# Kernel tuning notes

Measured on AMD Instinct MI355X. Metric: run time of the kernel, lower is better.

The kernel has to match this reference:

```python
import jax, jax.numpy as jnp
from jax import lax
import numpy as np

N, C, H, W = 8, 256, 96, 96
K = 5            # d_conv=4 forced odd -> 5 in FauxScan1D
HID = 2 * C      # ff_mult * dim


def setup_inputs() -> dict:
    key = jax.random.key(0)
    ks = iter(jax.random.split(key, 40))
    nrm = lambda *s: jax.random.normal(next(ks), s, jnp.float32) * 0.02
    inp = {'x': jax.random.normal(next(ks), (N, C, H, W), jnp.float32)}
    inp['ln1_w'] = jnp.ones((C,), jnp.float32)
    inp['ln1_b'] = jnp.zeros((C,), jnp.float32)
    inp['dw_w'] = nrm(3, 3, 1, C)   # depthwise 3x3, HWIO with feature_group_count=C
    inp['dw_b'] = jnp.zeros((C,), jnp.float32)
    for d in ('lr', 'rl', 'tb', 'bt'):
        inp[d + '_dw_w'] = nrm(K, 1, C)   # depthwise conv1d, WIO
        inp[d + '_dw_b'] = jnp.zeros((C,), jnp.float32)
        inp[d + '_g_w'] = nrm(C, C)       # 1x1 gate conv (out, in)
        inp[d + '_g_b'] = jnp.zeros((C,), jnp.float32)
    inp['fuse_w'] = nrm(C, C)
    inp['fuse_b'] = jnp.zeros((C,), jnp.float32)
    inp['ln2_w'] = jnp.ones((C,), jnp.float32)
    inp['ln2_b'] = jnp.zeros((C,), jnp.float32)
    inp['ff1_w'] = nrm(2 * HID, C)
    inp['ff1_b'] = jnp.zeros((2 * HID,), jnp.float32)
    inp['ff2_w'] = nrm(C, HID)
    inp['ff2_b'] = jnp.zeros((C,), jnp.float32)
    return inp


def _ln2d(x, w, b, eps=1e-6):
    # LayerNorm2d: per-(sample, channel) stats over H,W
    m = x.mean(axis=(2, 3), keepdims=True)
    v = ((x - m) ** 2).mean(axis=(2, 3), keepdims=True)
    return (x - m) * lax.rsqrt(v + eps) * w[None, :, None, None] + b[None, :, None, None]


def _scan1d(seq, dw_w, dw_b, g_w, g_b):
    # FauxScan1D: seq (B, L, C) -> dwconv1d(k=5, pad=2) * sigmoid(pointwise gate)
    c = seq.shape[-1]
    y = lax.conv_general_dilated(seq, dw_w, (1,), [(K // 2, K // 2)],
                                 dimension_numbers=('NWC', 'WIO', 'NWC'),
                                 feature_group_count=c) + dw_b
    g = jax.nn.sigmoid(jnp.einsum('blc,dc->bld', seq, g_w) + g_b)
    return y * g


def _forward(x, ln1_w, ln1_b, dw_w, dw_b,
             lr_dw_w, lr_dw_b, lr_g_w, lr_g_b,
             rl_dw_w, rl_dw_b, rl_g_w, rl_g_b,
             tb_dw_w, tb_dw_b, tb_g_w, tb_g_b,
             bt_dw_w, bt_dw_b, bt_g_w, bt_g_b,
             fuse_w, fuse_b, ln2_w, ln2_b, ff1_w, ff1_b, ff2_w, ff2_b):
    n, c, hh, ww = x.shape
    y = _ln2d(x, ln1_w, ln1_b)
    y = lax.conv_general_dilated(y, dw_w, (1, 1), [(1, 1), (1, 1)],
                                 dimension_numbers=('NCHW', 'HWIO', 'NCHW'),
                                 feature_group_count=c) + dw_b[None, :, None, None]
    y = jnp.transpose(y, (0, 2, 3, 1))  # NHWC
    # lr: rows as sequences
    o = _scan1d(y.reshape(n * hh, ww, c), lr_dw_w, lr_dw_b, lr_g_w, lr_g_b).reshape(n, hh, ww, c)
    # rl: flip width, scan, flip back
    yf = jnp.flip(y, 2).reshape(n * hh, ww, c)
    o = o + jnp.flip(_scan1d(yf, rl_dw_w, rl_dw_b, rl_g_w, rl_g_b).reshape(n, hh, ww, c), 2)
    # tb: columns as sequences
    yt = jnp.transpose(y, (0, 2, 1, 3)).reshape(n * ww, hh, c)
    o = o + jnp.transpose(_scan1d(yt, tb_dw_w, tb_dw_b, tb_g_w, tb_g_b).reshape(n, ww, hh, c), (0, 2, 1, 3))
    # bt: flip height, columns, scan, undo
    yb = jnp.transpose(jnp.flip(y, 1), (0, 2, 1, 3)).reshape(n * ww, hh, c)
    o = o + jnp.flip(jnp.transpose(_scan1d(yb, bt_dw_w, bt_dw_b, bt_g_w, bt_g_b).reshape(n, ww, hh, c), (0, 2, 1, 3)), 1)
    y = jnp.transpose(o, (0, 3, 1, 2))  # back to NCHW
    y = jnp.einsum('nchw,dc->ndhw', y, fuse_w) + fuse_b[None, :, None, None]
    x = x + y
    z = _ln2d(x, ln2_w, ln2_b)
    z = jnp.einsum('nchw,dc->ndhw', z, ff1_w) + ff1_b[None, :, None, None]
    a, g = jnp.split(z, 2, axis=1)  # GLU on channel dim
    z = a * jax.nn.sigmoid(g)
    z = jnp.einsum('nchw,dc->ndhw', z, ff2_w) + ff2_b[None, :, None, None]
    return x + z


def reference(x, ln1_w, ln1_b, dw_w, dw_b,
              lr_dw_w, lr_dw_b, lr_g_w, lr_g_b,
              rl_dw_w, rl_dw_b, rl_g_w, rl_g_b,
              tb_dw_w, tb_dw_b, tb_g_w, tb_g_b,
              bt_dw_w, bt_dw_b, bt_g_w, bt_g_b,
              fuse_w, fuse_b, ln2_w, ln2_b, ff1_w, ff1_b, ff2_w, ff2_b):
    return _forward(x, ln1_w, ln1_b, dw_w, dw_b,
                    lr_dw_w, lr_dw_b, lr_g_w, lr_g_b,
                    rl_dw_w, rl_dw_b, rl_g_w, rl_g_b,
                    tb_dw_w, tb_dw_b, tb_g_w, tb_g_b,
                    bt_dw_w, bt_dw_b, bt_g_w, bt_g_b,
                    fuse_w, fuse_b, ln2_w, ln2_b, ff1_w, ff1_b, ff2_w, ff2_b)
```

## Files before the change

### kernel.cpp

```cpp
#include <hip/hip_runtime.h>

#define TPB 256
#define HWSZ 9216

typedef __attribute__((ext_vector_type(8))) short short8x;
typedef __attribute__((ext_vector_type(4))) float f32x4;
typedef unsigned short ushort_t;
typedef unsigned int uint_t;

__device__ __forceinline__ float sigf(float v) { return 1.0f / (1.0f + __expf(-v)); }

__device__ __forceinline__ ushort_t f2bf(float f) {
  uint_t u = __float_as_uint(f);
  u = (u + 0x7fffu + ((u >> 16) & 1u)) >> 16;
  return (ushort_t)u;
}
__device__ __forceinline__ float bf2f(ushort_t h) {
  return __uint_as_float(((uint_t)h) << 16);
}

__device__ __forceinline__ int swz32(int p, int c) {
  return p * 1024 + ((((c * 4) ^ ((p & 7) << 4)) ^ (((p >> 3) & 3) << 2)));
}

__global__ __launch_bounds__(TPB) void k_pack(
    const float* __restrict__ lrg, const float* __restrict__ rlg,
    const float* __restrict__ tbg, const float* __restrict__ btg,
    const float* __restrict__ fusew, const float* __restrict__ ff1w,
    const float* __restrict__ ff2w,
    ushort_t* __restrict__ Gp, ushort_t* __restrict__ Ftp,
    ushort_t* __restrict__ W1p, ushort_t* __restrict__ W2p) {
  int i = blockIdx.x * TPB + threadIdx.x;
  if (i < 262144) {
    int d = i >> 16, r = i & 65535;
    int kt = r >> 13, nt = (r >> 9) & 15, l = (r >> 3) & 63, j = r & 7;
    int k = kt * 32 + (l >> 4) * 8 + j;
    int n_ = nt * 16 + (l & 15);
    const float* g = (d == 0) ? lrg : (d == 1) ? rlg : (d == 2) ? tbg : btg;
    Gp[i] = f2bf(g[n_ * 256 + k]);
  } else if (i < 327680) {
    int r = i - 262144;
    int kt = r >> 13, nt = (r >> 9) & 15, l = (r >> 3) & 63, j = r & 7;
    int k = kt * 32 + (l >> 4) * 8 + j;
    int n_ = nt * 16 + (l & 15);
    Ftp[r] = f2bf(fusew[n_ * 256 + k]);
  } else if (i < 589824) {
    int r = i - 327680;
    int kt = r >> 15, pb = (r >> 10) & 31, ag = (r >> 9) & 1;
    int l = (r >> 3) & 63, j = r & 7;
    int k = kt * 32 + (l >> 4) * 8 + j;
    int colb = pb * 16 + (l & 15);
    int col = ag ? (512 + colb) : colb;
    W1p[r] = f2bf(ff1w[col * 256 + k]);
  } else if (i < 720896) {
    int r = i - 589824;
    int kt = r >> 13, nt = (r >> 9) & 15, l = (r >> 3) & 63, j = r & 7;
    int k = kt * 32 + (l >> 4) * 8 + j;
    int n_ = nt * 16 + (l & 15);
    W2p[r] = f2bf(ff2w[n_ * 512 + k]);
  }
}

__global__ __launch_bounds__(TPB) void k_stats(const float* __restrict__ src,
                                               float* __restrict__ mean,
                                               float* __restrict__ rstd) {
  int nc = blockIdx.x;
  const float4* p = (const float4*)(src + (long)nc * HWSZ);
  float s = 0.f, s2 = 0.f;
  for (int i = threadIdx.x; i < 2304; i += TPB) {
    float4 v = p[i];
    s += (v.x + v.y) + (v.z + v.w);
    s2 = fmaf(v.x, v.x, fmaf(v.y, v.y, fmaf(v.z, v.z, fmaf(v.w, v.w, s2))));
  }
#pragma unroll
  for (int off = 32; off > 0; off >>= 1) {
    s += __shfl_down(s, off);
    s2 += __shfl_down(s2, off);
  }
  __shared__ float ls[4], ls2[4];
  int lane = threadIdx.x & 63, wv = threadIdx.x >> 6;
  if (lane == 0) { ls[wv] = s; ls2[wv] = s2; }
  __syncthreads();
  if (threadIdx.x == 0) {
    float S = ls[0] + ls[1] + ls[2] + ls[3];
    float S2 = ls2[0] + ls2[1] + ls2[2] + ls2[3];
    float m = S * (1.0f / HWSZ);
    float var = S2 * (1.0f / HWSZ) - m * m;
    mean[nc] = m;
    rstd[nc] = rsqrtf(fmaxf(var, 0.f) + 1e-6f);
  }
}

__global__ __launch_bounds__(TPB) void k_lndw(
    const float* __restrict__ x, const float* __restrict__ mean1,
    const float* __restrict__ rstd1, const float* __restrict__ ln1w,
    const float* __restrict__ ln1b, const float* __restrict__ dww,
    const float* __restrict__ dwb, ushort_t* __restrict__ y,
    ushort_t* __restrict__ yT) {
  __shared__ __align__(16) ushort_t xs[6 * 32 * 104];
  __shared__ __align__(16) ushort_t ot[2 * 96 * 32];
  __shared__ float sc[32], sh[32];

  int tid = threadIdx.x;
  int bid = blockIdx.x;
  int cb = (bid & 7) * 32;
  int hb = (bid >> 3) % 24;
  int n  = bid / 192;
  int h0 = hb * 4;

  if (tid < 32) {
    int c = cb + tid;
    int nc = n * 256 + c;
    float scale = rstd1[nc] * ln1w[c];
    sc[tid] = scale;
    sh[tid] = ln1b[c] - mean1[nc] * scale;
  }
  if (tid < 192) {
    xs[tid * 104 + 3] = 0;
    xs[tid * 104 + 100] = 0;
  }
  __syncthreads();

  for (int i = tid; i < 4608; i += TPB) {
    int rc = i / 24;
    int f4 = i - rc * 24;
    int row = rc >> 5, c = rc & 31;
    int hh = h0 - 1 + row;
    uint2 pk = make_uint2(0, 0);
    if (hh >= 0 && hh < 96) {
      float4 v = *(const float4*)(x + (long)(n * 256 + cb + c) * HWSZ +
                                  hh * 96 + f4 * 4);
      float scale = sc[c], shift = sh[c];
      ushort_t p0 = f2bf(fmaf(v.x, scale, shift));
      ushort_t p1 = f2bf(fmaf(v.y, scale, shift));
      ushort_t p2 = f2bf(fmaf(v.z, scale, shift));
      ushort_t p3 = f2bf(fmaf(v.w, scale, shift));
      pk.x = (uint_t)p0 | ((uint_t)p1 << 16);
      pk.y = (uint_t)p2 | ((uint_t)p3 << 16);
    }
    *(uint2*)(xs + rc * 104 + 4 + f4 * 4) = pk;
  }
  __syncthreads();

  int c = tid & 31, grp = tid >> 5;
  int w0 = grp * 12;
  float wgt[9];
#pragma unroll
  for (int t = 0; t < 9; ++t) wgt[t] = dww[t * 256 + cb + c];
  float bias = dwb[cb + c];

#pragma unroll
  for (int half = 0; half < 2; ++half) {
    float vals[2][12];
#pragma unroll
    for (int sub = 0; sub < 2; ++sub) {
      int orow = half * 2 + sub;
      float R[3][14];
#pragma unroll
      for (int rr = 0; rr < 3; ++rr) {
        const ushort_t* p = xs + ((orow + rr) * 32 + c) * 104;
        R[rr][0] = bf2f(p[3 + w0]);
        ushort4 q0 = *(const ushort4*)(p + 4 + w0);
        ushort4 q1 = *(const ushort4*)(p + 8 + w0);
        ushort4 q2 = *(const ushort4*)(p + 12 + w0);
        R[rr][1] = bf2f(q0.x);  R[rr][2] = bf2f(q0.y);
        R[rr][3] = bf2f(q0.z);  R[rr][4] = bf2f(q0.w);
        R[rr][5] = bf2f(q1.x);  R[rr][6] = bf2f(q1.y);
        R[rr][7] = bf2f(q1.z);  R[rr][8] = bf2f(q1.w);
        R[rr][9] = bf2f(q2.x);  R[rr][10] = bf2f(q2.y);
        R[rr][11] = bf2f(q2.z); R[rr][12] = bf2f(q2.w);
        R[rr][13] = bf2f(p[16 + w0]);
      }
#pragma unroll
      for (int k = 0; k < 12; ++k) {
        float acc = bias;
#pragma unroll
        for (int rr = 0; rr < 3; ++rr) {
          acc = fmaf(R[rr][k], wgt[rr * 3 + 0], acc);
          acc = fmaf(R[rr][k + 1], wgt[rr * 3 + 1], acc);
          acc = fmaf(R[rr][k + 2], wgt[rr * 3 + 2], acc);
        }
        vals[sub][k] = acc;
      }
    }
    if (half == 1) __syncthreads();
#pragma unroll
    for (int sub = 0; sub < 2; ++sub)
#pragma unroll
      for (int k = 0; k < 12; ++k)
        ot[(sub * 96 + w0 + k) * 32 + c] = f2bf(vals[sub][k]);
    __syncthreads();
#pragma unroll
    for (int it = 0; it < 3; ++it) {
      int u = it * 256 + tid;
      int r2 = (u >= 384) ? 1 : 0;
      int rem = u - r2 * 384;
      int w = rem >> 2, cq = rem & 3;
      uint4 v = *(const uint4*)(ot + (r2 * 96 + w) * 32 + cq * 8);
      int h = h0 + half * 2 + r2;
      *(uint4*)(y + ((long)(n * 96 + h) * 96 + w) * 256 + cb + cq * 8) = v;
      *(uint4*)(yT + ((long)(n * 96 + w) * 96 + h) * 256 + cb + cq * 8) = v;
    }
  }
}

__global__ __launch_bounds__(512, 4) void k_scan(
    const ushort_t* __restrict__ src, const uint4* __restrict__ gp4,
    const float* __restrict__ dwaw, const float* __restrict__ dwab,
    const float* __restrict__ gab, const float* __restrict__ dwbw,
    const float* __restrict__ dwbb, const float* __restrict__ gbb,
    ushort_t* __restrict__ dst) {
  __shared__ __align__(16) char pool[34816];
  char* ylds = pool;
  char* olds = pool + 26624;

  int tid = threadIdx.x;
  int bid = blockIdx.x;
  int seg = bid & 1, line = (bid >> 1) % 96, n = bid / 192;
  int p0 = seg * 48;
  long lbase = (long)(n * 96 + line) * 96;

  for (int u = tid; u < 52 * 32; u += 512) {
    int r = u >> 5, ks = u & 31;
    int q = p0 - 2 + r;
    uint4 v = make_uint4(0, 0, 0, 0);
    if (q >= 0 && q < 96)
      v = *(const uint4*)(src + (lbase + q) * 256 + ks * 8);
    *(uint4*)(ylds + r * 512 + ((ks * 16) ^ ((r & 7) << 4))) = v;
  }
  __syncthreads();

  int l = tid & 63, w = tid >> 6;
  int llo = l & 15, lhi = l >> 4;

  float part[3][2][4];

#pragma unroll
  for (int diri = 0; diri < 2; ++diri) {
    f32x4 acc[3][2];
#pragma unroll
    for (int mf = 0; mf < 3; ++mf)
#pragma unroll
      for (int ntl = 0; ntl < 2; ++ntl) acc[mf][ntl] = (f32x4){0.f, 0.f, 0.f, 0.f};

    const uint4* gbase = gp4 + ((long)(diri * 8) * 16 + w * 2) * 64 + l;
    short8x bc0 = *(const short8x*)(gbase);
    short8x bc1 = *(const short8x*)(gbase + 64);
#pragma unroll
    for (int kt = 0; kt < 8; ++kt) {
      short8x bn0, bn1;
      if (kt < 7) {
        bn0 = *(const short8x*)(gbase + (kt + 1) * 1024);
        bn1 = *(const short8x*)(gbase + (kt + 1) * 1024 + 64);
      }
      short8x a[3];
#pragma unroll
      for (int mf = 0; mf < 3; ++mf) {
        int arow = 2 + mf * 16 + llo;
        a[mf] = *(const short8x*)(ylds + arow * 512 +
                                  ((kt * 64 + lhi * 16) ^ ((arow & 7) << 4)));
      }
#pragma unroll
      for (int mf = 0; mf < 3; ++mf) {
        acc[mf][0] = __builtin_amdgcn_mfma_f32_16x16x32_bf16(a[mf], bc0, acc[mf][0], 0, 0, 0);
        acc[mf][1] = __builtin_amdgcn_mfma_f32_16x16x32_bf16(a[mf], bc1, acc[mf][1], 0, 0, 0);
      }
      bc0 = bn0;
      bc1 = bn1;
    }

    const float* dwv = diri ? dwbw : dwaw;
    const float* dbv = diri ? dwbb : dwab;
    const float* gbv = diri ? gbb : gab;
#pragma unroll
    for (int ntl = 0; ntl < 2; ++ntl) {
      int c = (w * 2 + ntl) * 16 + llo;
      float wt[5];
#pragma unroll
      for (int t = 0; t < 5; ++t)
        wt[t] = diri ? dwv[(4 - t) * 256 + c] : dwv[t * 256 + c];
      float cb = dbv[c], gb = gbv[c];
#pragma unroll
      for (int mf = 0; mf < 3; ++mf) {
        int pbase = mf * 16 + lhi * 4;
        float yv[8];
#pragma unroll
        for (int t = 0; t < 8; ++t) {
          int ry = pbase + t;
          yv[t] = bf2f(*(const ushort_t*)(ylds + ry * 512 +
                                          ((c * 2) ^ ((ry & 7) << 4))));
        }
#pragma unroll
        for (int r = 0; r < 4; ++r) {
          float conv = cb;
#pragma unroll
          for (int t = 0; t < 5; ++t) conv = fmaf(yv[r + t], wt[t], conv);
          float val = conv * sigf(acc[mf][ntl][r] + gb);
          if (diri == 0) part[mf][ntl][r] = val;
          else           part[mf][ntl][r] += val;
        }
      }
    }
  }

#pragma unroll
  for (int mf = 0; mf < 3; ++mf) {
    __syncthreads();
#pragma unroll
    for (int ntl = 0; ntl < 2; ++ntl) {
      int c = (w * 2 + ntl) * 16 + llo;
#pragma unroll
      for (int r = 0; r < 4; ++r) {
        int p = lhi * 4 + r;
        *(ushort_t*)(olds + p * 512 + ((c * 2) ^ ((p & 7) << 4))) =
            f2bf(part[mf][ntl][r]);
      }
    }
    __syncthreads();
    {
      int p = tid >> 5, ks = tid & 31;
      uint4 v = *(const uint4*)(olds + p * 512 + ((ks * 16) ^ ((p & 7) << 4)));
      *(uint4*)(dst + (lbase + p0 + mf * 16 + p) * 256 + ks * 8) = v;
    }
  }
}

__global__ __launch_bounds__(512, 4) void k_fuse(
    const ushort_t* __restrict__ o, const ushort_t* __restrict__ oT,
    const ushort_t* __restrict__ Ftp, const float* __restrict__ fuseb,
    const float* __restrict__ x, float* __restrict__ out) {
  __shared__ __align__(16) char pool[24576];

  int tid = threadIdx.x;
  int pix0 = blockIdx.x * 48;
  int n = pix0 / HWSZ, hw0 = pix0 % HWSZ;
  int h = hw0 / 96, w0 = hw0 % 96;

  for (int u = tid; u < 48 * 32; u += 512) {
    int r = u >> 5, ks = u & 31;
    uint4 va = *(const uint4*)(o + (long)(pix0 + r) * 256 + ks * 8);
    uint4 vb = *(const uint4*)(oT + ((long)(n * 96 + w0 + r) * 96 + h) * 256 + ks * 8);
    ushort_t* a8 = (ushort_t*)&va;
    ushort_t* b8 = (ushort_t*)&vb;
#pragma unroll
    for (int j = 0; j < 8; ++j) a8[j] = f2bf(bf2f(a8[j]) + bf2f(b8[j]));
    *(uint4*)(pool + r * 512 + ((ks * 16) ^ ((r & 7) << 4))) = va;
  }
  __syncthreads();

  int l = tid & 63, w = tid >> 6;
  int llo = l & 15, lhi = l >> 4;

  const uint4* fp4 = (const uint4*)Ftp;
  f32x4 acc[3][2];
#pragma unroll
  for (int mf = 0; mf < 3; ++mf)
#pragma unroll
    for (int ntl = 0; ntl < 2; ++ntl) acc[mf][ntl] = (f32x4){0.f, 0.f, 0.f, 0.f};

  const uint4* fbase = fp4 + (long)(w * 2) * 64 + l;
  short8x bc0 = *(const short8x*)(fbase);
  short8x bc1 = *(const short8x*)(fbase + 64);
#pragma unroll
  for (int kt = 0; kt < 8; ++kt) {
    short8x bn0, bn1;
    if (kt < 7) {
      bn0 = *(const short8x*)(fbase + (kt + 1) * 1024);
      bn1 = *(const short8x*)(fbase + (kt + 1) * 1024 + 64);
    }
    short8x a[3];
#pragma unroll
    for (int mf = 0; mf < 3; ++mf) {
      int arow = mf * 16 + llo;
      a[mf] = *(const short8x*)(pool + arow * 512 +
                                ((kt * 64 + lhi * 16) ^ ((arow & 7) << 4)));
    }
#pragma unroll
    for (int mf = 0; mf < 3; ++mf) {
      acc[mf][0] = __builtin_amdgcn_mfma_f32_16x16x32_bf16(a[mf], bc0, acc[mf][0], 0, 0, 0);
      acc[mf][1] = __builtin_amdgcn_mfma_f32_16x16x32_bf16(a[mf], bc1, acc[mf][1], 0, 0, 0);
    }
    bc0 = bn0;
    bc1 = bn1;
  }

#pragma unroll
  for (int mf = 0; mf < 3; ++mf) {
    __syncthreads();
#pragma unroll
    for (int ntl = 0; ntl < 2; ++ntl) {
      int c = (w * 2 + ntl) * 16 + llo;
      float fb = fuseb[c];
#pragma unroll
      for (int r = 0; r < 4; ++r) {
        int p = lhi * 4 + r;
        *(float*)(pool + swz32(p, c)) = acc[mf][ntl][r] + fb;
      }
    }
    __syncthreads();
    for (int i = tid; i < 4096; i += 512) {
      int c = i >> 4, p = i & 15;
      long addr = (long)(n * 256 + c) * HWSZ + hw0 + mf * 16 + p;
      out[addr] = x[addr] + *(const float*)(pool + swz32(p, c));
    }
  }
}

__global__ __launch_bounds__(512, 4) void k_ff1(
    const float* __restrict__ xres, const float* __restrict__ mean2,
    const float* __restrict__ rstd2, const float* __restrict__ ln2w,
    const float* __restrict__ ln2b, const ushort_t* __restrict__ W1p,
    const float* __restrict__ ff1b, ushort_t* __restrict__ u) {
  __shared__ char hA[48 * 512];

  int tid = threadIdx.x;
  int pix0 = blockIdx.x * 48;
  int n = pix0 / HWSZ, hw0 = pix0 % HWSZ;

  for (int i = tid; i < 12288; i += 512) {
    int c = i / 48, p = i % 48;
    int nc = n * 256 + c;
    float v = xres[(long)nc * HWSZ + hw0 + p];
    float hv = (v - mean2[nc]) * rstd2[nc] * ln2w[c] + ln2b[c];
    *(ushort_t*)(hA + p * 512 + ((c * 2) ^ ((p & 7) << 4))) = f2bf(hv);
  }
  __syncthreads();

  int l = tid & 63, w = tid >> 6;
  int llo = l & 15, lhi = l >> 4;

  const uint4* W1p4 = (const uint4*)W1p;
#pragma unroll
  for (int q = 0; q < 4; ++q) {
    int pb = q * 8 + w;
    f32x4 ca[3][2];
#pragma unroll
    for (int mf = 0; mf < 3; ++mf) {
      ca[mf][0] = (f32x4){0.f, 0.f, 0.f, 0.f};
      ca[mf][1] = (f32x4){0.f, 0.f, 0.f, 0.f};
    }
    const uint4* wb = W1p4 + (long)(pb * 2) * 64 + l;
    short8x bca = *(const short8x*)(wb);
    short8x bcg = *(const short8x*)(wb + 64);
#pragma unroll
    for (int kt = 0; kt < 8; ++kt) {
      short8x bna, bng;
      if (kt < 7) {
        bna = *(const short8x*)(wb + (kt + 1) * 4096);
        bng = *(const short8x*)(wb + (kt + 1) * 4096 + 64);
      }
      short8x a[3];
#pragma unroll
      for (int mf = 0; mf < 3; ++mf) {
        int arow = mf * 16 + llo;
        a[mf] = *(const short8x*)(hA + arow * 512 +
                                  ((kt * 64 + lhi * 16) ^ ((arow & 7) << 4)));
      }
#pragma unroll
      for (int mf = 0; mf < 3; ++mf) {
        ca[mf][0] = __builtin_amdgcn_mfma_f32_16x16x32_bf16(a[mf], bca, ca[mf][0], 0, 0, 0);
        ca[mf][1] = __builtin_amdgcn_mfma_f32_16x16x32_bf16(a[mf], bcg, ca[mf][1], 0, 0, 0);
      }
      bca = bna;
      bcg = bng;
    }
    int ucol = pb * 16 + llo;
    float ba = ff1b[ucol], bg = ff1b[512 + ucol];
#pragma unroll
    for (int mf = 0; mf < 3; ++mf)
#pragma unroll
      for (int r = 0; r < 4; ++r) {
        int row = pix0 + mf * 16 + lhi * 4 + r;
        u[(long)row * 512 + ucol] =
            f2bf((ca[mf][0][r] + ba) * sigf(ca[mf][1][r] + bg));
      }
  }
}

__global__ __launch_bounds__(512, 4) void k_ff2(
    const ushort_t* __restrict__ u, const ushort_t* __restrict__ W2p,
    const float* __restrict__ ff2b, float* __restrict__ out) {
  __shared__ __align__(16) char pool[16384];

  int tid = threadIdx.x;
  int pix0 = blockIdx.x * 48;
  int n = pix0 / HWSZ, hw0 = pix0 % HWSZ;

  int l = tid & 63, w = tid >> 6;
  int llo = l & 15, lhi = l >> 4;

  const uint4* W2p4 = (const uint4*)W2p;
  const uint_t* u32 = (const uint_t*)u;

  f32x4 zacc[3][2];
#pragma unroll
  for (int mf = 0; mf < 3; ++mf) {
    zacc[mf][0] = (f32x4){0.f, 0.f, 0.f, 0.f};
    zacc[mf][1] = (f32x4){0.f, 0.f, 0.f, 0.f};
  }

#pragma unroll
  for (int kc = 0; kc < 4; ++kc) {
    __syncthreads();
    for (int i = tid; i < 3072; i += 512) {
      int p = i >> 6, cd = i & 63;
      uint_t v = u32[(long)(pix0 + p) * 256 + kc * 64 + cd];
      *(uint_t*)(pool + p * 256 + ((cd * 4) ^ ((p & 7) << 4))) = v;
    }
    __syncthreads();
#pragma unroll
    for (int ks = 0; ks < 4; ++ks) {
      int kt = kc * 4 + ks;
      short8x a[3];
#pragma unroll
      for (int mf = 0; mf < 3; ++mf) {
        int arow = mf * 16 + llo;
        a[mf] = *(const short8x*)(pool + arow * 256 +
                                  ((ks * 64 + lhi * 16) ^ ((arow & 7) << 4)));
      }
      short8x b0 = *(const short8x*)(W2p4 + (long)(kt * 16 + w * 2) * 64 + l);
      short8x b1 = *(const short8x*)(W2p4 + (long)(kt * 16 + w * 2 + 1) * 64 + l);
#pragma unroll
      for (int mf = 0; mf < 3; ++mf) {
        zacc[mf][0] = __builtin_amdgcn_mfma_f32_16x16x32_bf16(a[mf], b0, zacc[mf][0], 0, 0, 0);
        zacc[mf][1] = __builtin_amdgcn_mfma_f32_16x16x32_bf16(a[mf], b1, zacc[mf][1], 0, 0, 0);
      }
    }
  }

#pragma unroll
  for (int mf = 0; mf < 3; ++mf) {
    __syncthreads();
#pragma unroll
    for (int ntl = 0; ntl < 2; ++ntl) {
      int c = (w * 2 + ntl) * 16 + llo;
      float fb = ff2b[c];
#pragma unroll
      for (int r = 0; r < 4; ++r) {
        int p = lhi * 4 + r;
        *(float*)(pool + swz32(p, c)) = zacc[mf][ntl][r] + fb;
      }
    }
    __syncthreads();
    for (int i = tid; i < 4096; i += 512) {
      int c = i >> 4, p = i & 15;
      long addr = (long)(n * 256 + c) * HWSZ + hw0 + mf * 16 + p;
      out[addr] += *(const float*)(pool + swz32(p, c));
    }
  }
}

extern "C" void kernel_launch(void* const* d_in, const int* in_sizes, int n_in,
                              void* d_out, int out_size, void* d_ws, size_t ws_size,
                              hipStream_t stream) {
  (void)in_sizes; (void)n_in; (void)out_size; (void)ws_size;
  const float* x     = (const float*)d_in[0];
  const float* ln1w  = (const float*)d_in[1];
  const float* ln1b  = (const float*)d_in[2];
  const float* dww   = (const float*)d_in[3];
  const float* dwb   = (const float*)d_in[4];
  const float* lr_w  = (const float*)d_in[5];
  const float* lr_b  = (const float*)d_in[6];
  const float* lr_gw = (const float*)d_in[7];
  const float* lr_gb = (const float*)d_in[8];
  const float* rl_w  = (const float*)d_in[9];
  const float* rl_b  = (const float*)d_in[10];
  const float* rl_gw = (const float*)d_in[11];
  const float* rl_gb = (const float*)d_in[12];
  const float* tb_w  = (const float*)d_in[13];
  const float* tb_b  = (const float*)d_in[14];
  const float* tb_gw = (const float*)d_in[15];
  const float* tb_gb = (const float*)d_in[16];
  const float* bt_w  = (const float*)d_in[17];
  const float* bt_b  = (const float*)d_in[18];
  const float* bt_gw = (const float*)d_in[19];
  const float* bt_gb = (const float*)d_in[20];
  const float* fusew = (const float*)d_in[21];
  const float* fuseb = (const float*)d_in[22];
  const float* ln2w  = (const float*)d_in[23];
  const float* ln2b  = (const float*)d_in[24];
  const float* ff1w  = (const float*)d_in[25];
  const float* ff1b  = (const float*)d_in[26];
  const float* ff2w  = (const float*)d_in[27];
  const float* ff2b  = (const float*)d_in[28];

  float* out = (float*)d_out;
  ushort_t* y  = (ushort_t*)d_ws;
  ushort_t* yT = y + 18874368;
  ushort_t* o  = yT + 18874368;
  ushort_t* oT = o + 18874368;
  ushort_t* uu = y;
  float* mean1 = (float*)(oT + 18874368);
  float* rstd1 = mean1 + 2048;
  float* mean2 = rstd1 + 2048;
  float* rstd2 = mean2 + 2048;
  ushort_t* Gp  = (ushort_t*)(rstd2 + 2048);
  ushort_t* Ftp = Gp + 262144;
  ushort_t* W1p = Ftp + 65536;
  ushort_t* W2p = W1p + 262144;

  k_pack<<<2816, TPB, 0, stream>>>(lr_gw, rl_gw, tb_gw, bt_gw, fusew, ff1w, ff2w,
                                   Gp, Ftp, W1p, W2p);
  k_stats<<<2048, TPB, 0, stream>>>(x, mean1, rstd1);
  k_lndw<<<1536, TPB, 0, stream>>>(x, mean1, rstd1, ln1w, ln1b, dww, dwb, y, yT);
  k_scan<<<1536, 512, 0, stream>>>(y, (const uint4*)Gp,
                                   lr_w, lr_b, lr_gb, rl_w, rl_b, rl_gb, o);
  k_scan<<<1536, 512, 0, stream>>>(yT, (const uint4*)(Gp + 131072),
                                   tb_w, tb_b, tb_gb, bt_w, bt_b, bt_gb, oT);
  k_fuse<<<1536, 512, 0, stream>>>(o, oT, Ftp, fuseb, x, out);
  k_stats<<<2048, TPB, 0, stream>>>(out, mean2, rstd2);
  k_ff1<<<1536, 512, 0, stream>>>(out, mean2, rstd2, ln2w, ln2b, W1p, ff1b, uu);
  k_ff2<<<1536, 512, 0, stream>>>(uu, W2p, ff2b, out);
}
```

Baseline: 363.1 us.

## Vectorize LN2 staging and store GLU intermediate in 4-row packed layout

The ff1 kernel now precomputes per-channel LayerNorm scale and shift in shared memory and loads the residual as float2 pairs across two channels, writing packed bf16 pairs to LDS. The GLU output u is stored in a blocked layout where each column holds 4 consecutive rows packed into a uint2, so each lane writes 8 bytes instead of four scattered 2-byte stores. ff2 reads that packed layout with uint2 loads and scatters the halves into its swizzled LDS tile. The aim is fewer, wider global transactions and less per-element arithmetic, at the cost of 2-byte LDS scatter stores in ff2.

```diff
diff --git a/kernel.cpp b/kernel.cpp
--- a/kernel.cpp
+++ b/kernel.cpp
@@ -412,17 +412,35 @@
     const float* __restrict__ ln2b, const ushort_t* __restrict__ W1p,
     const float* __restrict__ ff1b, ushort_t* __restrict__ u) {
   __shared__ char hA[48 * 512];
+  __shared__ float sc[256], sh[256];
 
   int tid = threadIdx.x;
   int pix0 = blockIdx.x * 48;
   int n = pix0 / HWSZ, hw0 = pix0 % HWSZ;
 
-  for (int i = tid; i < 12288; i += 512) {
-    int c = i / 48, p = i % 48;
-    int nc = n * 256 + c;
-    float v = xres[(long)nc * HWSZ + hw0 + p];
-    float hv = (v - mean2[nc]) * rstd2[nc] * ln2w[c] + ln2b[c];
-    *(ushort_t*)(hA + p * 512 + ((c * 2) ^ ((p & 7) << 4))) = f2bf(hv);
+  if (tid < 256) {
+    int nc = n * 256 + tid;
+    float scale = rstd2[nc] * ln2w[tid];
+    sc[tid] = scale;
+    sh[tid] = ln2b[tid] - mean2[nc] * scale;
+  }
+  __syncthreads();
+
+  for (int i = tid; i < 3072; i += 512) {
+    int cp = i / 24, pp = i % 24;
+    int c0 = cp * 2;
+    long base0 = (long)(n * 256 + c0) * HWSZ + hw0 + pp * 2;
+    float2 v0 = *(const float2*)(xres + base0);
+    float2 v1 = *(const float2*)(xres + base0 + HWSZ);
+    float s0 = sc[c0], h0 = sh[c0];
+    float s1 = sc[c0 + 1], h1 = sh[c0 + 1];
+    int p0 = pp * 2;
+    uint_t w0 = (uint_t)f2bf(fmaf(v0.x, s0, h0)) |
+                ((uint_t)f2bf(fmaf(v1.x, s1, h1)) << 16);
+    uint_t w1 = (uint_t)f2bf(fmaf(v0.y, s0, h0)) |
+                ((uint_t)f2bf(fmaf(v1.y, s1, h1)) << 16);
+    *(uint_t*)(hA + p0 * 512 + ((c0 * 2) ^ ((p0 & 7) << 4))) = w0;
+    *(uint_t*)(hA + (p0 + 1) * 512 + ((c0 * 2) ^ (((p0 + 1) & 7) << 4))) = w1;
   }
   __syncthreads();
 
@@ -466,14 +484,18 @@
     }
     int ucol = pb * 16 + llo;
     float ba = ff1b[ucol], bg = ff1b[512 + ucol];
-#pragma unroll
-    for (int mf = 0; mf < 3; ++mf)
-#pragma unroll
-      for (int r = 0; r < 4; ++r) {
-        int row = pix0 + mf * 16 + lhi * 4 + r;
-        u[(long)row * 512 + ucol] =
-            f2bf((ca[mf][0][r] + ba) * sigf(ca[mf][1][r] + bg));
-      }
+    int rb0 = (pix0 >> 2) + lhi;
+#pragma unroll
+    for (int mf = 0; mf < 3; ++mf) {
+      ushort_t b0 = f2bf((ca[mf][0][0] + ba) * sigf(ca[mf][1][0] + bg));
+      ushort_t b1 = f2bf((ca[mf][0][1] + ba) * sigf(ca[mf][1][1] + bg));
+      ushort_t b2 = f2bf((ca[mf][0][2] + ba) * sigf(ca[mf][1][2] + bg));
+      ushort_t b3 = f2bf((ca[mf][0][3] + ba) * sigf(ca[mf][1][3] + bg));
+      uint2 pk;
+      pk.x = (uint_t)b0 | ((uint_t)b1 << 16);
+      pk.y = (uint_t)b2 | ((uint_t)b3 << 16);
+      *(uint2*)(u + ((long)(rb0 + mf * 4) * 512 + ucol) * 4) = pk;
+    }
   }
 }
 
@@ -485,12 +507,12 @@
   int tid = threadIdx.x;
   int pix0 = blockIdx.x * 48;
   int n = pix0 / HWSZ, hw0 = pix0 % HWSZ;
+  int rb0 = pix0 >> 2;
 
   int l = tid & 63, w = tid >> 6;
   int llo = l & 15, lhi = l >> 4;
 
   const uint4* W2p4 = (const uint4*)W2p;
-  const uint_t* u32 = (const uint_t*)u;
 
   f32x4 zacc[3][2];
 #pragma unroll
@@ -502,10 +524,14 @@
 #pragma unroll
   for (int kc = 0; kc < 4; ++kc) {
     __syncthreads();
-    for (int i = tid; i < 3072; i += 512) {
-      int p = i >> 6, cd = i & 63;
-      uint_t v = u32[(long)(pix0 + p) * 256 + kc * 64 + cd];
-      *(uint_t*)(pool + p * 256 + ((cd * 4) ^ ((p & 7) << 4))) = v;
+    for (int i = tid; i < 1536; i += 512) {
+      int col = i & 127, rbl = i >> 7;
+      uint2 v = *(const uint2*)(u + ((long)(rb0 + rbl) * 512 + kc * 128 + col) * 4);
+      ushort_t* b = (ushort_t*)&v;
+      int p = rbl * 4;
+#pragma unroll
+      for (int k = 0; k < 4; ++k)
+        *(ushort_t*)(pool + (p + k) * 256 + ((col * 2) ^ (((p + k) & 7) << 4))) = b[k];
     }
     __syncthreads();
 #pragma unroll
```

Result: faster. 344.8 us, median of 2 (-5.0%).
